# Kernel tuning notes

Hardware: AMD Instinct MI355X
Metric: run time of the kernel (lower is better)

The kernel has to match this reference:

```python
import jax, jax.numpy as jnp
import numpy as np

N_NODES = 100000


def _gcn_edges(edge_index, num_nodes):
    # Add self-loops and compute symmetric GCN normalization per edge.
    src = jnp.concatenate([edge_index[0], jnp.arange(num_nodes, dtype=edge_index.dtype)])
    dst = jnp.concatenate([edge_index[1], jnp.arange(num_nodes, dtype=edge_index.dtype)])
    deg = jnp.zeros((num_nodes,), jnp.float32).at[dst].add(1.0)
    dinv = jnp.where(deg > 0, jax.lax.rsqrt(deg), 0.0)
    norm = dinv[src] * dinv[dst]  # [E+N]
    return src, dst, norm


def _gcn_conv(x, W, b, src, dst, norm, num_nodes):
    h = x @ W                         # [N, d_out] transform first (d_out <= d_in)
    msg = h[src] * norm[:, None]      # [E, d_out] gather + scale
    agg = jax.ops.segment_sum(msg, dst, num_segments=num_nodes)
    return agg + b


def setup_inputs() -> dict:
    key = jax.random.key(0)
    k = jax.random.split(key, 8)
    n, e, d_in, d_out = N_NODES, 1600000, 128, 64
    hid = 2 * d_out
    s = lambda fan: 1.0 / np.sqrt(fan)
    return {
        "x": jax.random.normal(k[0], (n, d_in), jnp.float32),
        "edge_index": jax.random.randint(k[1], (2, e), 0, n, jnp.int64),
        "W1": jax.random.normal(k[2], (d_in, hid), jnp.float32) * s(d_in),
        "b1": jnp.zeros((hid,), jnp.float32),
        "Wmu": jax.random.normal(k[3], (hid, d_out), jnp.float32) * s(hid),
        "bmu": jnp.zeros((d_out,), jnp.float32),
        "Wls": jax.random.normal(k[4], (hid, d_out), jnp.float32) * s(hid),
        "bls": jnp.zeros((d_out,), jnp.float32),
    }


def reference(x, edge_index, W1, b1, Wmu, bmu, Wls, bls):
    n = x.shape[0]
    src, dst, norm = _gcn_edges(edge_index, n)
    h = jax.nn.relu(_gcn_conv(x, W1, b1, src, dst, norm, n))
    mu = _gcn_conv(h, Wmu, bmu, src, dst, norm, n)
    logstd = _gcn_conv(h, Wls, bls, src, dst, norm, n)
    return mu, logstd
```

## Files before the change

kernel.cpp:

```cpp
#include <hip/hip_runtime.h>

#define DIN 128
#define HID 128
#define DOUT 64
#define NCHUNK 784
#define BSH 9
#define NB1MAX 256
#define BSLACK 1540

typedef unsigned short ushort_t;
typedef unsigned int uint_t;
typedef __attribute__((ext_vector_type(4))) short s4v;
typedef __attribute__((ext_vector_type(4))) float f4v;

#if defined(__has_builtin)
#if __has_builtin(__builtin_amdgcn_mfma_f32_16x16x16bf16_1k)
#define MFMA16(a, b, c) __builtin_amdgcn_mfma_f32_16x16x16bf16_1k(a, b, c, 0, 0, 0)
#endif
#endif
#ifndef MFMA16
static __device__ inline f4v mfma16_asm(s4v a, s4v b, f4v c) {
  asm volatile("v_mfma_f32_16x16x16_bf16 %0, %1, %2, %0" : "+v"(c) : "v"(a), "v"(b));
  return c;
}
#define MFMA16(a, b, c) mfma16_asm(a, b, c)
#endif

static inline int ceil_div(int a, int b) { return (a + b - 1) / b; }

__device__ inline ushort_t f2bf(float f) {
  uint_t u = __float_as_uint(f);
  u += 0x7fff + ((u >> 16) & 1);
  return (ushort_t)(u >> 16);
}
__device__ inline uint_t pack2bf(float a, float b) {
  return (uint_t)f2bf(a) | ((uint_t)f2bf(b) << 16);
}
__device__ inline float2 bf2x2(uint_t u) {
  return make_float2(__uint_as_float(u << 16), __uint_as_float(u & 0xffff0000u));
}

__device__ inline int blk_scan_incl(int v, int* ws, int nw) {
  int t = threadIdx.x, lane = t & 63, w = t >> 6;
#pragma unroll
  for (int d = 1; d < 64; d <<= 1) {
    int u = __shfl_up(v, d, 64);
    if (lane >= d) v += u;
  }
  if (lane == 63) ws[w] = v;
  __syncthreads();
  if (w == 0) {
    int s = (lane < nw) ? ws[lane] : 0;
    for (int d = 1; d < nw; d <<= 1) {
      int u = __shfl_up(s, d, 64);
      if (lane >= d) s += u;
    }
    if (lane < nw) ws[lane] = s;
  }
  __syncthreads();
  if (w > 0) v += ws[w - 1];
  return v;
}


__global__ __launch_bounds__(512) void k_setup(const int* __restrict__ dst, int E, int CH,
                                               int nb1, int* __restrict__ counts,
                                               const float* __restrict__ x,
                                               const float* __restrict__ W1,
                                               const float* __restrict__ Wmu,
                                               const float* __restrict__ Wls,
                                               ushort_t* __restrict__ Wt2,
                                               ushort_t* __restrict__ xWb,
                                               ushort_t* __restrict__ h,
                                               float* __restrict__ dinv, int N, int G1) {
  __shared__ ushort_t Ws[128][132];
  __shared__ uint_t cnt[NB1MAX];
  int b = blockIdx.x, t = threadIdx.x;
  if (b < G1) {
#pragma unroll
    for (int it = 0; it < 16; it++) {
      int k = it * 8 + ((t >> 7) << 1);
      int j = t & 127;
      float a = W1[k * 128 + j];
      float bb = W1[(k + 1) * 128 + j];
      *(uint_t*)&Ws[j][k] = pack2bf(a, bb);
    }
    __syncthreads();
    int w = t >> 6, lane = t & 63;
    int rl = lane & 15, g = lane >> 4;
    int row = b * 128 + w * 16 + rl;
    bool valid = row < N;
    const float* Ar = x + (size_t)row * DIN + 4 * g;
    s4v af[8];
#pragma unroll
    for (int kk = 0; kk < 8; kk++) {
      float4 v = make_float4(0.f, 0.f, 0.f, 0.f);
      if (valid) v = *(const float4*)(Ar + kk * 16);
      s4v a;
      a[0] = (short)f2bf(v.x);
      a[1] = (short)f2bf(v.y);
      a[2] = (short)f2bf(v.z);
      a[3] = (short)f2bf(v.w);
      af[kk] = a;
    }
    f4v acc[8];
#pragma unroll
    for (int ct = 0; ct < 8; ct++) acc[ct] = (f4v)0.f;
#pragma unroll
    for (int kk = 0; kk < 8; kk++) {
      int ko = kk * 16 + 4 * g;
#pragma unroll
      for (int ct = 0; ct < 8; ct++) {
        s4v bb = *(s4v*)&Ws[ct * 16 + rl][ko];
        acc[ct] = MFMA16(af[kk], bb, acc[ct]);
      }
    }
    int gr0 = b * 128 + w * 16 + 4 * g;
#pragma unroll
    for (int i = 0; i < 4; i++) {
      int gr = gr0 + i;
      if (gr < N) {
#pragma unroll
        for (int ct = 0; ct < 8; ct++)
          xWb[(size_t)gr * HID + ct * 16 + rl] = f2bf(acc[ct][i]);
      }
    }
  } else if (b < G1 + NCHUNK) {
    int c = b - G1;
    for (int i = t; i < nb1; i += 512) cnt[i] = 0;
    __syncthreads();
    int e0 = c * CH, e1 = min(E, e0 + CH);
    for (int i = e0 + t; i < e1; i += 512) atomicAdd(&cnt[((uint_t)dst[i]) >> BSH], 1u);
    __syncthreads();
    for (int i = t; i < nb1; i += 512) counts[c * nb1 + i] = (int)cnt[i];
  } else if (b < G1 + NCHUNK + 32) {
    int idx = (b - G1 - NCHUNK) * 512 + t;
    int j = idx >> 7, k = idx & 127;
    Wt2[j * 128 + k] = f2bf(j < 64 ? Wmu[k * 64 + j] : Wls[k * 64 + (j - 64)]);
  } else {
    if (t < 64) ((uint_t*)(xWb + (size_t)N * HID))[t] = 0;
    else if (t < 128) ((uint_t*)(h + (size_t)N * HID))[t - 64] = 0;
    else if (t == 128) dinv[N] = 0.f;
  }
}

__global__ __launch_bounds__(256) void k_bscan(const int* __restrict__ counts, int nb1,
                                               int* __restrict__ chunk_off,
                                               int* __restrict__ btot) {
  __shared__ int ws[8];
  __shared__ int shc;
  int b = blockIdx.x, t = threadIdx.x;
  int carry = 0;
#pragma unroll
  for (int r = 0; r < NCHUNK / 256 + 1; r++) {
    int idx = r * 256 + t;
    int v = (idx < NCHUNK) ? counts[idx * nb1 + b] : 0;
    int incl = blk_scan_incl(v, ws, 4) + carry;
    if (idx < NCHUNK) chunk_off[idx * nb1 + b] = incl - v;
    if (t == 255) shc = incl;
    __syncthreads();
    carry = shc;
  }
  if (t == 0) btot[b] = carry;
}

__global__ __launch_bounds__(256) void k_bscatter(const int* __restrict__ src,
                                                  const int* __restrict__ dst, int E, int CH,
                                                  int nb1, const int* __restrict__ btot,
                                                  const int* __restrict__ chunk_off,
                                                  uint_t* __restrict__ tmp) {
  __shared__ int ws[8];
  __shared__ uint_t cur[NB1MAX];
  int t = threadIdx.x, c = blockIdx.x;
  {
    int v = (t < nb1) ? btot[t] : 0;
    int incl = blk_scan_incl(v, ws, 4);
    if (t < nb1) cur[t] = (uint_t)(incl - v + chunk_off[c * nb1 + t]);
  }
  __syncthreads();
  int e0 = c * CH, e1 = min(E, e0 + CH);
  for (int i = e0 + t; i < e1; i += 256) {
    uint_t d = (uint_t)dst[i];
    uint_t s = (uint_t)src[i];
    uint_t p = atomicAdd(&cur[d >> BSH], 1u);
    tmp[p] = ((d & ((1u << BSH) - 1)) << 17) | s;
  }
}

__global__ __launch_bounds__(512) void k_bfinal(const uint_t* __restrict__ tmp,
                                                const int* __restrict__ btot, int N, int nb1,
                                                uint_t* __restrict__ csr,
                                                int* __restrict__ row_ptr,
                                                int* __restrict__ row_end,
                                                float* __restrict__ dinv) {
  __shared__ int ws[8];
  __shared__ int sseg0, sseg1;
  __shared__ uint_t cnt[1 << BSH];
  __shared__ uint_t ppfx[1 << BSH];
  __shared__ uint_t cur[1 << BSH];
  int b = blockIdx.x, t = threadIdx.x;
  {
    int v = (t < nb1) ? btot[t] : 0;
    int incl = blk_scan_incl(v, ws, 8);
    if (t == b) {
      sseg0 = incl - v;
      sseg1 = incl;
    }
  }
  for (int i = t; i < (1 << BSH); i += 512) cnt[i] = 0;
  __syncthreads();
  int seg0 = sseg0, seg1 = sseg1;
  int pb = ((seg0 + 3) & ~3) + BSLACK * b;
  for (int i = seg0 + t; i < seg1; i += 512) atomicAdd(&cnt[tmp[i] >> 17], 1u);
  __syncthreads();
  if (t < 64) {
    uint_t pc[8];
    uint_t s = 0;
#pragma unroll
    for (int k = 0; k < 8; k++) {
      pc[k] = (cnt[t * 8 + k] + 3u) & ~3u;
      s += pc[k];
    }
    int incl = (int)s;
#pragma unroll
    for (int d = 1; d < 64; d <<= 1) {
      int u = __shfl_up(incl, d, 64);
      if (t >= d) incl += u;
    }
    uint_t excl = (uint_t)incl - s;
#pragma unroll
    for (int k = 0; k < 8; k++) {
      ppfx[t * 8 + k] = excl;
      excl += pc[k];
    }
  }
  __syncthreads();
  int nd0 = b << BSH;
  for (int i = t; i < (1 << BSH); i += 512) {
    cur[i] = ppfx[i];
    int g = nd0 + i;
    if (g < N) {
      row_ptr[g] = pb + (int)ppfx[i];
      row_end[g] = pb + (int)(ppfx[i] + ((cnt[i] + 3u) & ~3u));
      dinv[g] = rsqrtf((float)cnt[i] + 1.0f);
    }
  }
  __syncthreads();
  for (int i = seg0 + t; i < seg1; i += 512) {
    uint_t v = tmp[i];
    uint_t pos = atomicAdd(&cur[v >> 17], 1u);
    csr[pb + (int)pos] = v & 0x1FFFFu;
  }
  __syncthreads();
  for (int i = t; i < (1 << BSH); i += 512) {
    uint_t e0 = cur[i];
    uint_t e1 = ppfx[i] + ((cnt[i] + 3u) & ~3u);
    for (uint_t k = e0; k < e1; k++) csr[pb + (int)k] = (uint_t)N;
  }
}


__global__ __launch_bounds__(256) void k_agg1(const ushort_t* __restrict__ H,
                                              const int* __restrict__ row_ptr,
                                              const int* __restrict__ row_end,
                                              const uint_t* __restrict__ csr,
                                              const float* __restrict__ dinv,
                                              const float* __restrict__ bias,
                                              ushort_t* __restrict__ out, int n) {
  int node = (blockIdx.x * blockDim.x + threadIdx.x) >> 6;
  int lane = threadIdx.x & 63;
  if (node >= n) return;
  const char* Hb = (const char*)H;
  const char* Db = (const char*)dinv;
  uint_t loff = (uint_t)lane << 2;
  float dn = dinv[node];
  int j = row_ptr[node], end = row_end[node];
  float2 hs = bf2x2(*(const uint_t*)(Hb + ((size_t)(((uint_t)node << 8) | loff))));
  float ax = dn * hs.x, ay = dn * hs.y;
  if (j < end) {
    uint4 c = *(const uint4*)(csr + j);
    while (true) {
      int jn = j + 4;
      bool more = jn < end;
      uint4 cn;
      if (more) cn = *(const uint4*)(csr + jn);
      float w0 = *(const float*)(Db + (size_t)(c.x << 2));
      float w1 = *(const float*)(Db + (size_t)(c.y << 2));
      float w2 = *(const float*)(Db + (size_t)(c.z << 2));
      float w3 = *(const float*)(Db + (size_t)(c.w << 2));
      uint_t v0 = *(const uint_t*)(Hb + (size_t)((c.x << 8) | loff));
      uint_t v1 = *(const uint_t*)(Hb + (size_t)((c.y << 8) | loff));
      uint_t v2 = *(const uint_t*)(Hb + (size_t)((c.z << 8) | loff));
      uint_t v3 = *(const uint_t*)(Hb + (size_t)((c.w << 8) | loff));
      float2 f0 = bf2x2(v0), f1 = bf2x2(v1), f2 = bf2x2(v2), f3 = bf2x2(v3);
      ax += w0 * f0.x; ay += w0 * f0.y;
      ax += w1 * f1.x; ay += w1 * f1.y;
      ax += w2 * f2.x; ay += w2 * f2.y;
      ax += w3 * f3.x; ay += w3 * f3.y;
      if (!more) break;
      c = cn;
      j = jn;
    }
  }
  ax = fmaxf(dn * ax + bias[2 * lane], 0.f) * dn;
  ay = fmaxf(dn * ay + bias[2 * lane + 1], 0.f) * dn;
  ((uint_t*)out)[(size_t)node * 64 + lane] = pack2bf(ax, ay);
}


__global__ __launch_bounds__(256) void k_agg2(const ushort_t* __restrict__ H,
                                              const int* __restrict__ row_ptr,
                                              const int* __restrict__ row_end,
                                              const uint_t* __restrict__ csr,
                                              const float* __restrict__ dinv,
                                              ushort_t* __restrict__ out, int n) {
  int node = (blockIdx.x * blockDim.x + threadIdx.x) >> 6;
  int lane = threadIdx.x & 63;
  if (node >= n) return;
  const char* Hb = (const char*)H;
  uint_t loff = (uint_t)lane << 2;
  float dn = dinv[node];
  int j = row_ptr[node], end = row_end[node];
  float2 hs = bf2x2(*(const uint_t*)(Hb + ((size_t)(((uint_t)node << 8) | loff))));
  float ax = hs.x, ay = hs.y;
  if (j < end) {
    uint4 c = *(const uint4*)(csr + j);
    while (true) {
      int jn = j + 4;
      bool more = jn < end;
      uint4 cn;
      if (more) cn = *(const uint4*)(csr + jn);
      uint_t v0 = *(const uint_t*)(Hb + (size_t)((c.x << 8) | loff));
      uint_t v1 = *(const uint_t*)(Hb + (size_t)((c.y << 8) | loff));
      uint_t v2 = *(const uint_t*)(Hb + (size_t)((c.z << 8) | loff));
      uint_t v3 = *(const uint_t*)(Hb + (size_t)((c.w << 8) | loff));
      float2 f0 = bf2x2(v0), f1 = bf2x2(v1), f2 = bf2x2(v2), f3 = bf2x2(v3);
      ax += f0.x + f1.x;
      ay += f0.y + f1.y;
      ax += f2.x + f3.x;
      ay += f2.y + f3.y;
      if (!more) break;
      c = cn;
      j = jn;
    }
  }
  ax *= dn;
  ay *= dn;
  ((uint_t*)out)[(size_t)node * 64 + lane] = pack2bf(ax, ay);
}


__global__ __launch_bounds__(256) void k_gemm2(const ushort_t* __restrict__ A,
                                               const ushort_t* __restrict__ Wt,
                                               const float* __restrict__ bmu,
                                               const float* __restrict__ bls,
                                               float* __restrict__ out, int n) {
  __shared__ ushort_t Ws[128][132];
  int t = threadIdx.x;
#pragma unroll
  for (int i = 0; i < 16; i++) {
    int f = t + 256 * i;
    int rowj = f >> 5, seg = f & 31;
    *(uint2*)&Ws[rowj][seg * 4] = *(const uint2*)(Wt + rowj * 128 + seg * 4);
  }
  __syncthreads();
  int w = t >> 6, lane = t & 63;
  int rl = lane & 15, g = lane >> 4;
  int row = blockIdx.x * 64 + w * 16 + rl;
  bool valid = row < n;
  const ushort_t* Ar = A + (size_t)row * HID + 4 * g;
  s4v af[8];
#pragma unroll
  for (int kk = 0; kk < 8; kk++) {
    s4v a = (s4v)0;
    if (valid) a = *(const s4v*)(Ar + kk * 16);
    af[kk] = a;
  }
  f4v acc[8];
#pragma unroll
  for (int ct = 0; ct < 8; ct++) acc[ct] = (f4v)0.f;
#pragma unroll
  for (int kk = 0; kk < 8; kk++) {
    int ko = kk * 16 + 4 * g;
#pragma unroll
    for (int ct = 0; ct < 8; ct++) {
      s4v b = *(s4v*)&Ws[ct * 16 + rl][ko];
      acc[ct] = MFMA16(af[kk], b, acc[ct]);
    }
  }
  int gr0 = blockIdx.x * 64 + w * 16 + 4 * g;
#pragma unroll
  for (int ct = 0; ct < 8; ct++) {
    int col = ct * 16 + rl;
    float bv;
    size_t obase;
    int cc;
    if (ct < 4) {
      bv = bmu[col];
      obase = 0;
      cc = col;
    } else {
      bv = bls[col - 64];
      obase = (size_t)n * DOUT;
      cc = col - 64;
    }
#pragma unroll
    for (int i = 0; i < 4; i++) {
      int gr = gr0 + i;
      if (gr < n) out[obase + (size_t)gr * DOUT + cc] = acc[ct][i] + bv;
    }
  }
}


extern "C" void kernel_launch(void* const* d_in, const int* in_sizes, int n_in,
                              void* d_out, int out_size, void* d_ws, size_t ws_size,
                              hipStream_t stream) {
  const float* x   = (const float*)d_in[0];
  const int*   ei  = (const int*)d_in[1];
  const float* W1  = (const float*)d_in[2];
  const float* b1  = (const float*)d_in[3];
  const float* Wmu = (const float*)d_in[4];
  const float* bmu = (const float*)d_in[5];
  const float* Wls = (const float*)d_in[6];
  const float* bls = (const float*)d_in[7];
  float* out = (float*)d_out;

  const int N = in_sizes[0] / DIN;
  const int E = in_sizes[1] / 2;
  const int* esrc = ei;
  const int* edst = ei + E;
  const int nb1 = ceil_div(N, 1 << BSH);
  const int CH = ceil_div(E, NCHUNK);
  const int G1 = ceil_div(N, 128);

  char* ws = (char*)d_ws;
  size_t off = 0;
  auto alloc = [&](size_t bytes) -> void* {
    void* p = ws + off;
    off = (off + bytes + 255) & ~(size_t)255;
    return p;
  };
  ushort_t* xWb   = (ushort_t*)alloc((size_t)(N + 1) * HID * sizeof(ushort_t));
  ushort_t* h     = (ushort_t*)alloc((size_t)(N + 1) * HID * sizeof(ushort_t));
  uint_t* csr     = (uint_t*)alloc(((size_t)E + (size_t)(BSLACK + 8) * nb1 + 16) * 4);
  uint_t* tmp     = (uint_t*)alloc((size_t)E * 4);
  int* counts     = (int*)alloc((size_t)NCHUNK * nb1 * 4);
  int* chunk_off  = (int*)alloc((size_t)NCHUNK * nb1 * 4);
  int* btot       = (int*)alloc((size_t)nb1 * 4);
  int* row_ptr    = (int*)alloc((size_t)N * 4);
  int* row_end    = (int*)alloc((size_t)N * 4);
  float* dinv     = (float*)alloc((size_t)(N + 1) * 4);
  ushort_t* wt2b  = (ushort_t*)alloc((size_t)HID * HID * 2);
  (void)ws_size; (void)n_in; (void)out_size;

  k_setup<<<G1 + NCHUNK + 33, 512, 0, stream>>>(edst, E, CH, nb1, counts, x, W1, Wmu, Wls,
                                                wt2b, xWb, h, dinv, N, G1);
  k_bscan<<<nb1, 256, 0, stream>>>(counts, nb1, chunk_off, btot);
  k_bscatter<<<NCHUNK, 256, 0, stream>>>(esrc, edst, E, CH, nb1, btot, chunk_off, tmp);
  k_bfinal<<<nb1, 512, 0, stream>>>(tmp, btot, N, nb1, csr, row_ptr, row_end, dinv);

  k_agg1<<<ceil_div(N, 4), 256, 0, stream>>>(xWb, row_ptr, row_end, csr, dinv, b1, h, N);

  k_agg2<<<ceil_div(N, 4), 256, 0, stream>>>(h, row_ptr, row_end, csr, dinv, xWb, N);
  k_gemm2<<<ceil_div(N, 64), 256, 0, stream>>>(xWb, wt2b, bmu, bls, out, N);
}
```

Measured before the change: 214.0 us.

## Stage bucket scatter and CSR build in shared memory for coalesced writes

The bucket-scatter kernel now ranks each edge within its bucket locally, compacts the edges by bucket in LDS, and then writes contiguous runs to the global temp buffer, where it previously did scattered per-edge stores. The final CSR build kernel places edges into an LDS buffer pre-filled with padding and copies it out linearly, replacing scattered global stores and the serial padding loop. The intent is to remove uncoalesced global writes in the graph preprocessing. In exchange both kernels use much more LDS, which can lower occupancy, and the code assumes each chunk holds at most CHB*256 edges and each bucket's padded count fits in EBMAX.

```diff
diff --git a/kernel.cpp b/kernel.cpp
--- a/kernel.cpp
+++ b/kernel.cpp
@@ -4,9 +4,11 @@
 #define HID 128
 #define DOUT 64
 #define NCHUNK 784
+#define CHB 8
 #define BSH 9
 #define NB1MAX 256
 #define BSLACK 1540
+#define EBMAX 16384
 
 typedef unsigned short ushort_t;
 typedef unsigned int uint_t;
@@ -170,20 +172,57 @@
                                                   const int* __restrict__ chunk_off,
                                                   uint_t* __restrict__ tmp) {
   __shared__ int ws[8];
-  __shared__ uint_t cur[NB1MAX];
+  __shared__ uint_t cnt[NB1MAX];
+  __shared__ uint_t lofs[NB1MAX];
+  __shared__ uint_t gbase[NB1MAX];
+  __shared__ uint_t ebuf[CHB * 256];
+  __shared__ ushort_t bbuf[CHB * 256];
   int t = threadIdx.x, c = blockIdx.x;
   {
     int v = (t < nb1) ? btot[t] : 0;
     int incl = blk_scan_incl(v, ws, 4);
-    if (t < nb1) cur[t] = (uint_t)(incl - v + chunk_off[c * nb1 + t]);
+    if (t < nb1) {
+      gbase[t] = (uint_t)(incl - v + chunk_off[c * nb1 + t]);
+      cnt[t] = 0;
+    }
   }
   __syncthreads();
   int e0 = c * CH, e1 = min(E, e0 + CH);
-  for (int i = e0 + t; i < e1; i += 256) {
-    uint_t d = (uint_t)dst[i];
-    uint_t s = (uint_t)src[i];
-    uint_t p = atomicAdd(&cur[d >> BSH], 1u);
-    tmp[p] = ((d & ((1u << BSH) - 1)) << 17) | s;
+  int nloc = e1 - e0;
+  uint_t pay[CHB];
+  ushort_t bk[CHB], rk[CHB];
+#pragma unroll
+  for (int r = 0; r < CHB; r++) {
+    int i = e0 + r * 256 + t;
+    if (i < e1) {
+      uint_t d = (uint_t)dst[i];
+      uint_t s = (uint_t)src[i];
+      uint_t b = d >> BSH;
+      pay[r] = ((d & ((1u << BSH) - 1)) << 17) | s;
+      bk[r] = (ushort_t)b;
+      rk[r] = (ushort_t)atomicAdd(&cnt[b], 1u);
+    }
+  }
+  __syncthreads();
+  {
+    int v = (t < nb1) ? (int)cnt[t] : 0;
+    int incl = blk_scan_incl(v, ws, 4);
+    if (t < nb1) lofs[t] = (uint_t)(incl - v);
+  }
+  __syncthreads();
+#pragma unroll
+  for (int r = 0; r < CHB; r++) {
+    int i = e0 + r * 256 + t;
+    if (i < e1) {
+      uint_t p = lofs[bk[r]] + rk[r];
+      ebuf[p] = pay[r];
+      bbuf[p] = bk[r];
+    }
+  }
+  __syncthreads();
+  for (int i = t; i < nloc; i += 256) {
+    uint_t b = bbuf[i];
+    tmp[gbase[b] + ((uint_t)i - lofs[b])] = ebuf[i];
   }
 }
 
@@ -194,10 +233,11 @@
                                                 int* __restrict__ row_end,
                                                 float* __restrict__ dinv) {
   __shared__ int ws[8];
-  __shared__ int sseg0, sseg1;
+  __shared__ int sseg0, sseg1, sptot;
   __shared__ uint_t cnt[1 << BSH];
   __shared__ uint_t ppfx[1 << BSH];
   __shared__ uint_t cur[1 << BSH];
+  __shared__ uint_t ebuf[EBMAX];
   int b = blockIdx.x, t = threadIdx.x;
   {
     int v = (t < nb1) ? btot[t] : 0;
@@ -233,8 +273,10 @@
       ppfx[t * 8 + k] = excl;
       excl += pc[k];
     }
-  }
-  __syncthreads();
+    if (t == 63) sptot = (int)excl;
+  }
+  __syncthreads();
+  int ptot = sptot;
   int nd0 = b << BSH;
   for (int i = t; i < (1 << BSH); i += 512) {
     cur[i] = ppfx[i];
@@ -245,18 +287,15 @@
       dinv[g] = rsqrtf((float)cnt[i] + 1.0f);
     }
   }
+  for (int i = t; i < ptot; i += 512) ebuf[i] = (uint_t)N;
   __syncthreads();
   for (int i = seg0 + t; i < seg1; i += 512) {
     uint_t v = tmp[i];
     uint_t pos = atomicAdd(&cur[v >> 17], 1u);
-    csr[pb + (int)pos] = v & 0x1FFFFu;
-  }
-  __syncthreads();
-  for (int i = t; i < (1 << BSH); i += 512) {
-    uint_t e0 = cur[i];
-    uint_t e1 = ppfx[i] + ((cnt[i] + 3u) & ~3u);
-    for (uint_t k = e0; k < e1; k++) csr[pb + (int)k] = (uint_t)N;
-  }
+    ebuf[pos] = v & 0x1FFFFu;
+  }
+  __syncthreads();
+  for (int i = t; i < ptot; i += 512) csr[pb + i] = ebuf[i];
 }
 
 
```

Measured after the change: 205.4 us, median of 2. -4.0%, faster.
